# Optimization experiments

Measured on AMD Instinct MI355X. Metric: run time of the kernel, lower is better.

Reference implementation:

```python
import jax, jax.numpy as jnp
import numpy as np

NEG_SLOPE = 0.2


def gat_layer(x, src, dst, W, a_src, a_dst, num_nodes):
    """One PyG-style GATConv (self-loops already appended to src/dst).
    Returns [N, H, C] head-separated output (no bias/concat applied)."""
    H, C = a_src.shape
    h = (x @ W).reshape(num_nodes, H, C)            # [N,H,C]
    alpha_src = jnp.einsum('nhc,hc->nh', h, a_src)  # [N,H]
    alpha_dst = jnp.einsum('nhc,hc->nh', h, a_dst)  # [N,H]
    e = jax.nn.leaky_relu(alpha_src[src] + alpha_dst[dst], NEG_SLOPE)  # [E,H]
    # segment softmax over edges sharing the same destination node
    m = jax.ops.segment_max(e, dst, num_segments=num_nodes)[dst]
    ex = jnp.exp(e - m)
    denom = jax.ops.segment_sum(ex, dst, num_segments=num_nodes)[dst]
    alpha = ex / denom                               # [E,H]
    msg = h[src] * alpha[:, :, None]                 # [E,H,C]
    return jax.ops.segment_sum(msg, dst, num_segments=num_nodes)  # [N,H,C]


def setup_inputs() -> dict:
    key = jax.random.key(0)
    ks = jax.random.split(key, 10)
    N, E, IN, HID, OUT, H = 50000, 800000, 128, 32, 32, 4
    s = 0.1
    return {
        'x': jax.random.normal(ks[0], (N, IN), jnp.float32),
        'edge_index': jax.random.randint(ks[1], (2, E), 0, N, jnp.int64),
        'W1': jax.random.normal(ks[2], (IN, H * HID), jnp.float32) * s,
        'att_src1': jax.random.normal(ks[3], (H, HID), jnp.float32) * s,
        'att_dst1': jax.random.normal(ks[4], (H, HID), jnp.float32) * s,
        'b1': jax.random.normal(ks[5], (H * HID,), jnp.float32) * s,
        'W2': jax.random.normal(ks[6], (H * HID, OUT), jnp.float32) * s,
        'att_src2': jax.random.normal(ks[7], (1, OUT), jnp.float32) * s,
        'att_dst2': jax.random.normal(ks[8], (1, OUT), jnp.float32) * s,
        'b2': jax.random.normal(ks[9], (OUT,), jnp.float32) * s,
    }


def reference(x, edge_index, W1, att_src1, att_dst1, b1, W2, att_src2, att_dst2, b2):
    N = x.shape[0]
    # add self loops (PyG GATConv default)
    loop = jnp.arange(N, dtype=edge_index.dtype)
    src = jnp.concatenate([edge_index[0], loop])
    dst = jnp.concatenate([edge_index[1], loop])
    # layer 1: heads=4, concat=True
    h1 = gat_layer(x, src, dst, W1, att_src1, att_dst1, N).reshape(N, -1) + b1
    h1 = jax.nn.elu(h1)
    # layer 2: heads=1, concat=False -> mean over heads
    h2 = gat_layer(h1, src, dst, W2, att_src2, att_dst2, N).mean(axis=1) + b2
    return h2
```

## Files before the change

kernel.cpp:

```cpp
#include <hip/hip_runtime.h>
#include <math.h>

#define NEG_SLOPE 0.2f
typedef unsigned int uint;
typedef __attribute__((ext_vector_type(8))) short short8;
typedef __attribute__((ext_vector_type(4))) float floatx4;

__device__ __forceinline__ float lrelu(float x){ return x > 0.f ? x : NEG_SLOPE*x; }
__device__ __forceinline__ float sel4(float a,float b,float c,float d,int comp){
    return comp==0 ? a : (comp==1 ? b : (comp==2 ? c : d));
}
__device__ __forceinline__ uint f2bf(float f){
    uint u = __float_as_uint(f);
    return (u + 0x7FFFu + ((u>>16)&1u)) >> 16;
}
__device__ __forceinline__ float bf_lo(uint u){ return __uint_as_float(u<<16); }
__device__ __forceinline__ float bf_hi(uint u){ return __uint_as_float(u & 0xFFFF0000u); }
__device__ __forceinline__ float cexp(float x){ return __expf(fminf(x, 60.f)); }

__global__ __launch_bounds__(256) void k_prep(const float* __restrict__ W,
                                              ushort* __restrict__ wtb,
                                              int* __restrict__ offs, int N, int Etot)
{
    if (blockIdx.x == 0 && threadIdx.x == 0) offs[N] = Etot;
    int flat = blockIdx.x*1024 + threadIdx.x*4;
    int k = flat >> 7, c = flat & 127;
    float4 wv = *(const float4*)&W[flat];
    wtb[(size_t)(c+0)*128 + k] = (ushort)f2bf(wv.x);
    wtb[(size_t)(c+1)*128 + k] = (ushort)f2bf(wv.y);
    wtb[(size_t)(c+2)*128 + k] = (ushort)f2bf(wv.z);
    wtb[(size_t)(c+3)*128 + k] = (ushort)f2bf(wv.w);
}

__global__ __launch_bounds__(512) void k_g1b(const float* __restrict__ x,
    const ushort* __restrict__ wtb, uint* __restrict__ hb2, int N, int GB,
    const int* __restrict__ ei, int* __restrict__ bh, int E, int Etot, int NC, int NB)
{
    if (blockIdx.x >= GB){
        __shared__ uint hist[256];
        int c = blockIdx.x - GB;
        if (threadIdx.x < 256) hist[threadIdx.x] = 0;
        __syncthreads();
        int e0 = c*4096;
        #pragma unroll
        for (int r=0;r<8;r++){
            int e = e0 + r*512 + threadIdx.x;
            if (e < Etot){
                int d = (e < E) ? ei[E+e] : (e-E);
                atomicAdd(&hist[d>>8], 1u);
            }
        }
        __syncthreads();
        int b = threadIdx.x;
        if (b < NB) bh[(size_t)b*NC + c] = (int)hist[b];
        return;
    }
    __shared__ __align__(16) ushort xt[64][136];
    const int tid = threadIdx.x;
    const int row0 = blockIdx.x * 64;
    #pragma unroll
    for (int j=0;j<4;j++){
        int flat = j*2048 + tid*4;
        int r = flat >> 7, c = flat & 127;
        int gr = row0 + r;
        float4 xv = (gr < N) ? *(const float4*)&x[(size_t)gr*128 + c]
                             : make_float4(0.f,0.f,0.f,0.f);
        uint2 p;
        p.x = f2bf(xv.x) | (f2bf(xv.y)<<16);
        p.y = f2bf(xv.z) | (f2bf(xv.w)<<16);
        *(uint2*)&xt[r][c] = p;
    }
    __syncthreads();
    const int wv_ = tid >> 6, lane = tid & 63;
    const int l15 = lane & 15, hi = lane >> 4;
    const int rw = wv_ & 3, ch = wv_ >> 2;
    const int arow = rw*16 + l15;
    floatx4 acc[4];
    #pragma unroll
    for (int t=0;t<4;t++) acc[t] = (floatx4){0.f,0.f,0.f,0.f};
    #pragma unroll
    for (int ks=0; ks<4; ks++){
        short8 a = *(short8*)&xt[arow][ks*32 + hi*8];
        #pragma unroll
        for (int c4=0; c4<4; c4++){
            int ct = ch*4 + c4;
            short8 b = *(const short8*)&wtb[(size_t)(ct*16 + l15)*128 + ks*32 + hi*8];
            acc[c4] = __builtin_amdgcn_mfma_f32_16x16x32_bf16(a, b, acc[c4], 0, 0, 0);
        }
    }
    #pragma unroll
    for (int c4=0; c4<4; c4++){
        int ct = ch*4 + c4;
        #pragma unroll
        for (int r=0;r<4;r++){
            float v  = acc[c4][r];
            float pr = __shfl_xor(v, 1);
            int gr = row0 + rw*16 + (hi<<2) + r;
            if (((lane & 1) == 0) && gr < N)
                hb2[(size_t)gr*64 + ct*8 + (l15>>1)] = f2bf(v) | (f2bf(pr)<<16);
        }
    }
}

__global__ __launch_bounds__(256) void k_a1sc(const uint* __restrict__ hb2,
        const float* __restrict__ at_s, const float* __restrict__ at_d,
        float* __restrict__ as1, float* __restrict__ ad1, int N, int AB,
        const int* __restrict__ bh, int* __restrict__ bhs, int* __restrict__ partials2, int T)
{
    __shared__ int sm[256];
    if (blockIdx.x >= AB){
        int bid = blockIdx.x - AB;
        int tid = threadIdx.x;
        int i = bid*256 + tid;
        int v = (i < T) ? bh[i] : 0;
        sm[tid] = v;
        __syncthreads();
        for (int d=1; d<256; d<<=1){
            int t = (tid >= d) ? sm[tid-d] : 0;
            __syncthreads();
            sm[tid] += t;
            __syncthreads();
        }
        if (i < T) bhs[i] = sm[tid] - v;
        if (tid == 255) partials2[bid] = sm[255];
        return;
    }
    int wid = (blockIdx.x << 2) + (threadIdx.x >> 6);
    int lane = threadIdx.x & 63;
    if (wid >= N) return;
    uint hv = hb2[(size_t)wid*64 + lane];
    float f0 = bf_lo(hv), f1 = bf_hi(hv);
    float2 asv = *(const float2*)&at_s[2*lane];
    float2 adv = *(const float2*)&at_d[2*lane];
    float sa = f0*asv.x + f1*asv.y;
    float da = f0*adv.x + f1*adv.y;
    #pragma unroll
    for (int d=8; d>=1; d>>=1){ sa += __shfl_xor(sa,d); da += __shfl_xor(da,d); }
    if ((lane & 15) == 0){
        int head = lane >> 4;
        as1[(size_t)wid*4 + head] = sa;
        ad1[(size_t)wid*4 + head] = da;
    }
}

__global__ void k_bscan2s(int* __restrict__ bhs, const int* __restrict__ bh, int T){
    if (threadIdx.x == 0){
        int run = 0;
        for (int i=0;i<T;i++){ bhs[i] = run; run += bh[i]; }
    }
}

__global__ __launch_bounds__(256) void k_bscat(const int* __restrict__ ei,
        const int* __restrict__ bhs, const int* __restrict__ partials2, int L1e,
        uint* __restrict__ epack, int E, int Etot, int NC, int NB)
{
    __shared__ int sm[256];
    __shared__ int pbase[256];
    __shared__ uint cnt[256];
    int c = blockIdx.x, tid = threadIdx.x;
    int v = (tid < L1e) ? partials2[tid] : 0;
    sm[tid] = v;
    __syncthreads();
    for (int d=1; d<256; d<<=1){
        int t = (tid >= d) ? sm[tid-d] : 0;
        __syncthreads();
        sm[tid] += t;
        __syncthreads();
    }
    if (tid < NB){
        int i = tid*NC + c;
        int boff = (L1e == 0 || (i>>8) == 0) ? 0 : sm[(i>>8)-1];
        pbase[tid] = bhs[i] + boff;
    }
    cnt[tid] = 0;
    __syncthreads();
    int e0 = c*4096;
    #pragma unroll
    for (int r=0;r<16;r++){
        int e = e0 + r*256 + tid;
        if (e < Etot){
            int d, s;
            if (e < E){ s = ei[e]; d = ei[E+e]; }
            else      { s = e - E; d = e - E; }
            int b = d >> 8;
            uint lr = atomicAdd(&cnt[b], 1u);
            epack[pbase[b] + (int)lr] = (uint)s | ((uint)(d & 255) << 16);
        }
    }
}

__global__ __launch_bounds__(256) void k_bfin(const uint* __restrict__ epack,
        const int* __restrict__ bhs, const int* __restrict__ partials2, int L1e,
        int* __restrict__ bsrc, int* __restrict__ offs, int N, int NB, int NC, int Etot)
{
    __shared__ int sm[256];
    __shared__ int cnt[256], lofs[256], cnt2[256];
    int b = blockIdx.x, tid = threadIdx.x;
    int v = (tid < L1e) ? partials2[tid] : 0;
    sm[tid] = v;
    __syncthreads();
    for (int d=1; d<256; d<<=1){
        int t = (tid >= d) ? sm[tid-d] : 0;
        __syncthreads();
        sm[tid] += t;
        __syncthreads();
    }
    int i0 = b*NC;
    int start = bhs[i0] + ((L1e==0 || (i0>>8)==0) ? 0 : sm[(i0>>8)-1]);
    int end;
    if (b+1 < NB){
        int i1 = (b+1)*NC;
        end = bhs[i1] + ((L1e==0 || (i1>>8)==0) ? 0 : sm[(i1>>8)-1]);
    } else end = Etot;
    __syncthreads();
    cnt[tid] = 0; cnt2[tid] = 0;
    __syncthreads();
    for (int e = start + tid; e < end; e += 256)
        atomicAdd((uint*)&cnt[(epack[e] >> 16) & 255], 1u);
    __syncthreads();
    int v2 = cnt[tid];
    sm[tid] = v2;
    __syncthreads();
    for (int d=1; d<256; d<<=1){
        int t = (tid >= d) ? sm[tid-d] : 0;
        __syncthreads();
        sm[tid] += t;
        __syncthreads();
    }
    lofs[tid] = sm[tid] - v2;
    int nd = b*256 + tid;
    if (nd <= N) offs[nd] = start + sm[tid] - v2;
    __syncthreads();
    for (int e = start + tid; e < end; e += 256){
        uint u = epack[e];
        int dl = (u >> 16) & 255;
        int r = (int)atomicAdd((uint*)&cnt2[dl], 1u);
        bsrc[start + lofs[dl] + r] = (int)(u & 0xFFFFu);
    }
}

__global__ __launch_bounds__(512) void k_agg1(const uint* __restrict__ hb2,
    const float4* __restrict__ as1v, const float4* __restrict__ ad1v,
    const int* __restrict__ offs, const int* __restrict__ bsrc,
    const float* __restrict__ b1, float* __restrict__ exb,
    uint* __restrict__ hb1, int N)
{
    __shared__ float wsh[8][64][4];
    __shared__ int   ssh[8][64];
    int wv   = threadIdx.x >> 6;
    int wid  = (blockIdx.x << 3) + wv;
    int lane = threadIdx.x & 63;
    if (wid >= N) return;
    int base = offs[wid];
    int deg  = offs[wid+1] - base;
    float4 adv = ad1v[wid];
    const int comp = lane >> 4;
    float acc0=0.f, acc1=0.f;

    if (deg <= 64){
        const bool act = lane < deg;
        int sreg = 0;
        float e0=0.f,e1=0.f,e2=0.f,e3=0.f;
        if (act){
            sreg = bsrc[base+lane];
            float4 av = as1v[sreg];
            e0=cexp(lrelu(av.x+adv.x)); e1=cexp(lrelu(av.y+adv.y));
            e2=cexp(lrelu(av.z+adv.z)); e3=cexp(lrelu(av.w+adv.w));
        }
        float s0=e0,s1=e1,s2=e2,s3=e3;
        #pragma unroll
        for (int d=32; d>=1; d>>=1){
            s0+=__shfl_xor(s0,d); s1+=__shfl_xor(s1,d);
            s2+=__shfl_xor(s2,d); s3+=__shfl_xor(s3,d);
        }
        if (act){
            float i0=__builtin_amdgcn_rcpf(s0), i1=__builtin_amdgcn_rcpf(s1);
            float i2=__builtin_amdgcn_rcpf(s2), i3=__builtin_amdgcn_rcpf(s3);
            ssh[wv][lane]    = sreg << 6;
            wsh[wv][lane][0] = e0*i0;
            wsh[wv][lane][1] = e1*i1;
            wsh[wv][lane][2] = e2*i2;
            wsh[wv][lane][3] = e3*i3;
        }
        int j=0;
        for (; j+7 < deg; j+=8){
            uint o0=ssh[wv][j+0]+lane, o1=ssh[wv][j+1]+lane;
            uint o2=ssh[wv][j+2]+lane, o3=ssh[wv][j+3]+lane;
            uint o4=ssh[wv][j+4]+lane, o5=ssh[wv][j+5]+lane;
            uint o6=ssh[wv][j+6]+lane, o7=ssh[wv][j+7]+lane;
            float w0=wsh[wv][j+0][comp], w1=wsh[wv][j+1][comp];
            float w2=wsh[wv][j+2][comp], w3=wsh[wv][j+3][comp];
            float w4=wsh[wv][j+4][comp], w5=wsh[wv][j+5][comp];
            float w6=wsh[wv][j+6][comp], w7=wsh[wv][j+7][comp];
            uint h0=hb2[o0], h1_=hb2[o1], h2_=hb2[o2], h3=hb2[o3];
            uint h4=hb2[o4], h5=hb2[o5], h6=hb2[o6], h7=hb2[o7];
            acc0 = fmaf(bf_lo(h0), w0, acc0); acc1 = fmaf(bf_hi(h0), w0, acc1);
            acc0 = fmaf(bf_lo(h1_),w1, acc0); acc1 = fmaf(bf_hi(h1_),w1, acc1);
            acc0 = fmaf(bf_lo(h2_),w2, acc0); acc1 = fmaf(bf_hi(h2_),w2, acc1);
            acc0 = fmaf(bf_lo(h3), w3, acc0); acc1 = fmaf(bf_hi(h3), w3, acc1);
            acc0 = fmaf(bf_lo(h4), w4, acc0); acc1 = fmaf(bf_hi(h4), w4, acc1);
            acc0 = fmaf(bf_lo(h5), w5, acc0); acc1 = fmaf(bf_hi(h5), w5, acc1);
            acc0 = fmaf(bf_lo(h6), w6, acc0); acc1 = fmaf(bf_hi(h6), w6, acc1);
            acc0 = fmaf(bf_lo(h7), w7, acc0); acc1 = fmaf(bf_hi(h7), w7, acc1);
        }
        for (; j+3 < deg; j+=4){
            uint oA=ssh[wv][j]+lane,   oB=ssh[wv][j+1]+lane;
            uint oC=ssh[wv][j+2]+lane, oD=ssh[wv][j+3]+lane;
            float wA=wsh[wv][j][comp],   wB=wsh[wv][j+1][comp];
            float wC=wsh[wv][j+2][comp], wD=wsh[wv][j+3][comp];
            uint hA=hb2[oA], hB=hb2[oB], hC=hb2[oC], hD=hb2[oD];
            acc0 = fmaf(bf_lo(hA), wA, acc0); acc1 = fmaf(bf_hi(hA), wA, acc1);
            acc0 = fmaf(bf_lo(hB), wB, acc0); acc1 = fmaf(bf_hi(hB), wB, acc1);
            acc0 = fmaf(bf_lo(hC), wC, acc0); acc1 = fmaf(bf_hi(hC), wC, acc1);
            acc0 = fmaf(bf_lo(hD), wD, acc0); acc1 = fmaf(bf_hi(hD), wD, acc1);
        }
        for (; j < deg; j++){
            uint oA = ssh[wv][j]+lane;
            float wA = wsh[wv][j][comp];
            uint hA = hb2[oA];
            acc0 = fmaf(bf_lo(hA), wA, acc0);
            acc1 = fmaf(bf_hi(hA), wA, acc1);
        }
    } else {
        float s0=0,s1=0,s2=0,s3=0;
        for (int j=lane; j<deg; j+=64){
            int s = bsrc[base+j];
            float4 av = as1v[s];
            float e0=cexp(lrelu(av.x+adv.x));
            float e1=cexp(lrelu(av.y+adv.y));
            float e2=cexp(lrelu(av.z+adv.z));
            float e3=cexp(lrelu(av.w+adv.w));
            s0+=e0; s1+=e1; s2+=e2; s3+=e3;
            *(float4*)&exb[(size_t)(base+j)*4] = make_float4(e0,e1,e2,e3);
        }
        #pragma unroll
        for (int d=32; d>=1; d>>=1){
            s0+=__shfl_xor(s0,d); s1+=__shfl_xor(s1,d);
            s2+=__shfl_xor(s2,d); s3+=__shfl_xor(s3,d);
        }
        float invc = 1.0f / sel4(s0,s1,s2,s3,comp);
        for (int j=0;j<deg;j++){
            int s = bsrc[base+j];
            float w = exb[(size_t)(base+j)*4 + comp]*invc;
            uint hv = hb2[((uint)s<<6)+lane];
            acc0 = fmaf(bf_lo(hv), w, acc0);
            acc1 = fmaf(bf_hi(hv), w, acc1);
        }
    }
    float2 bv = *(const float2*)&b1[2*lane];
    float r0 = acc0 + bv.x;
    float r1 = acc1 + bv.y;
    r0 = r0 > 0.f ? r0 : (__expf(r0) - 1.f);
    r1 = r1 > 0.f ? r1 : (__expf(r1) - 1.f);
    hb1[(size_t)wid*64 + lane] = f2bf(r0) | (f2bf(r1)<<16);
}

__global__ __launch_bounds__(512) void k_l2pre(const uint* __restrict__ hb1,
    const float* __restrict__ W2, const float* __restrict__ asrc2,
    const float* __restrict__ adst2, uint* __restrict__ h2b,
    float* __restrict__ as2, float* __restrict__ ad2, int N)
{
    __shared__ __align__(16) float w2s[4096];
    __shared__ float a2s[32], a2d[32];
    int tid = threadIdx.x;
    #pragma unroll
    for (int q=0;q<2;q++){
        int idx = q*2048 + tid*4;
        *(float4*)&w2s[idx] = *(const float4*)&W2[idx];
    }
    if (tid < 32){ a2s[tid] = asrc2[tid]; a2d[tid] = adst2[tid]; }
    __syncthreads();
    int node = blockIdx.x*16 + (tid>>5);
    if (node >= N) return;
    int c = tid & 31;
    float acc = 0.f;
    #pragma unroll
    for (int k=0;k<128;k+=8){
        uint4 u = *(const uint4*)&hb1[(size_t)node*64 + (k>>1)];
        acc = fmaf(bf_lo(u.x), w2s[(k+0)*32+c], acc);
        acc = fmaf(bf_hi(u.x), w2s[(k+1)*32+c], acc);
        acc = fmaf(bf_lo(u.y), w2s[(k+2)*32+c], acc);
        acc = fmaf(bf_hi(u.y), w2s[(k+3)*32+c], acc);
        acc = fmaf(bf_lo(u.z), w2s[(k+4)*32+c], acc);
        acc = fmaf(bf_hi(u.z), w2s[(k+5)*32+c], acc);
        acc = fmaf(bf_lo(u.w), w2s[(k+6)*32+c], acc);
        acc = fmaf(bf_hi(u.w), w2s[(k+7)*32+c], acc);
    }
    float pr = __shfl_xor(acc, 1);
    if ((c & 1) == 0)
        h2b[(size_t)node*16 + (c>>1)] = f2bf(acc) | (f2bf(pr)<<16);
    float ps = acc * a2s[c], pd = acc * a2d[c];
    #pragma unroll
    for (int d=16; d>=1; d>>=1){ ps += __shfl_xor(ps,d); pd += __shfl_xor(pd,d); }
    if (c == 0){ as2[node] = ps; ad2[node] = pd; }
}

__global__ __launch_bounds__(512) void k_agg2(const uint* __restrict__ h2b,
    const float* __restrict__ as2, const float* __restrict__ ad2,
    const int* __restrict__ offs, const int* __restrict__ bsrc,
    const float* __restrict__ b2, float* __restrict__ exb,
    float* __restrict__ outp, int N)
{
    __shared__ float w2sh[8][64];
    __shared__ int   s2sh[8][64];
    int wv   = threadIdx.x >> 6;
    int wid  = (blockIdx.x << 3) + wv;
    int lane = threadIdx.x & 63;
    if (wid >= N) return;
    int base = offs[wid], deg = offs[wid+1] - base;
    float adn = ad2[wid];
    const int c2 = lane & 15, slot = lane >> 4;
    float acc0 = 0.f, acc1 = 0.f;

    if (deg <= 64){
        const bool act = lane < deg;
        int sreg = 0; float e = 0.f;
        if (act){ sreg = bsrc[base+lane]; e = cexp(lrelu(as2[sreg] + adn)); }
        float sum = e;
        #pragma unroll
        for (int d=32; d>=1; d>>=1) sum += __shfl_xor(sum,d);
        if (act){
            s2sh[wv][lane] = sreg << 4;
            w2sh[wv][lane] = e * __builtin_amdgcn_rcpf(sum);
        }
        int j = slot;
        for (; j+4 < deg; j += 8){
            uint oA = (uint)(s2sh[wv][j] + c2);
            uint oB = (uint)(s2sh[wv][j+4] + c2);
            float wA = w2sh[wv][j], wB = w2sh[wv][j+4];
            uint uA = h2b[oA], uB = h2b[oB];
            acc0 = fmaf(bf_lo(uA), wA, acc0); acc1 = fmaf(bf_hi(uA), wA, acc1);
            acc0 = fmaf(bf_lo(uB), wB, acc0); acc1 = fmaf(bf_hi(uB), wB, acc1);
        }
        for (; j < deg; j += 4){
            uint o  = (uint)(s2sh[wv][j] + c2);
            float w = w2sh[wv][j];
            uint u = h2b[o];
            acc0 = fmaf(bf_lo(u), w, acc0);
            acc1 = fmaf(bf_hi(u), w, acc1);
        }
    } else {
        float sum = 0.f;
        for (int j=lane; j<deg; j+=64){
            int s = bsrc[base+j];
            float ex = cexp(lrelu(as2[s] + adn));
            sum += ex;
            exb[base+j] = ex;
        }
        #pragma unroll
        for (int d=32; d>=1; d>>=1) sum += __shfl_xor(sum,d);
        float inv = 1.f/sum;
        for (int j=slot; j<deg; j+=4){
            int s  = bsrc[base+j];
            float w = exb[base+j]*inv;
            uint u = h2b[((uint)s<<4) + c2];
            acc0 = fmaf(bf_lo(u), w, acc0);
            acc1 = fmaf(bf_hi(u), w, acc1);
        }
    }
    acc0 += __shfl_xor(acc0, 16); acc0 += __shfl_xor(acc0, 32);
    acc1 += __shfl_xor(acc1, 16); acc1 += __shfl_xor(acc1, 32);
    if (lane < 16){
        float2 bv = *(const float2*)&b2[2*c2];
        *(float2*)&outp[(size_t)wid*32 + 2*c2] = make_float2(acc0 + bv.x, acc1 + bv.y);
    }
}

extern "C" void kernel_launch(void* const* d_in, const int* in_sizes, int n_in,
                              void* d_out, int out_size, void* d_ws, size_t ws_size,
                              hipStream_t stream)
{
    const float* x     = (const float*)d_in[0];
    const int*   ei    = (const int*)d_in[1];
    const float* W1    = (const float*)d_in[2];
    const float* at_s1 = (const float*)d_in[3];
    const float* at_d1 = (const float*)d_in[4];
    const float* b1    = (const float*)d_in[5];
    const float* W2    = (const float*)d_in[6];
    const float* at_s2 = (const float*)d_in[7];
    const float* at_d2 = (const float*)d_in[8];
    const float* b2    = (const float*)d_in[9];
    float* outp = (float*)d_out;

    const int N = in_sizes[0] / 128;
    const int E = in_sizes[1] / 2;
    const int Etot = E + N;

    const int NB = (N + 255) >> 8;
    const int NC = (Etot + 4095) / 4096;
    const int T  = NB * NC;
    const int L1 = (T + 255) / 256;

    float* f = (float*)d_ws;
    size_t off = 0;
    uint*  hb2 = (uint*)(f + off); off += (size_t)N*64;
    uint*  hb1 = (uint*)(f + off); off += (size_t)N*64;
    float* exb = f + off; off += (size_t)Etot*4;
    float* as1 = f + off; off += (size_t)N*4;
    float* ad1 = f + off; off += (size_t)N*4;
    uint*  h2b = (uint*)(f + off); off += (size_t)N*16;
    float* as2 = f + off; off += (size_t)N;
    float* ad2 = f + off; off += (size_t)N;
    ushort* wtb = (ushort*)(f + off); off += 8192;
    int* ib       = (int*)(f + off);
    int* offs     = ib;
    int* bh       = ib + N + 8;
    int* bhs      = bh + T;
    int* partials2= bhs + T;
    uint* epack   = (uint*)(partials2 + 256);
    int* bsrc     = (int*)(epack + Etot);

    const int GB = (N+63)/64;
    const int AB = (N+3)/4;

    k_prep <<<16, 256, 0, stream>>>(W1, wtb, offs, N, Etot);
    k_g1b  <<<GB+NC, 512, 0, stream>>>(x, wtb, hb2, N, GB, ei, bh, E, Etot, NC, NB);
    k_a1sc <<<AB+L1, 256, 0, stream>>>(hb2, at_s1, at_d1, as1, ad1, N, AB,
                                       bh, bhs, partials2, T);
    if (L1 <= 256){
        k_bscat<<<NC, 256, 0, stream>>>(ei, bhs, partials2, L1, epack, E, Etot, NC, NB);
        k_bfin <<<NB, 256, 0, stream>>>(epack, bhs, partials2, L1, bsrc, offs, N, NB, NC, Etot);
    } else {
        k_bscan2s<<<1, 1, 0, stream>>>(bhs, bh, T);
        k_bscat<<<NC, 256, 0, stream>>>(ei, bhs, partials2, 0, epack, E, Etot, NC, NB);
        k_bfin <<<NB, 256, 0, stream>>>(epack, bhs, partials2, 0, bsrc, offs, N, NB, NC, Etot);
    }
    k_agg1 <<<(N+7)/8, 512, 0, stream>>>(hb2, (const float4*)as1, (const float4*)ad1,
                                         offs, bsrc, b1, exb, hb1, N);
    k_l2pre<<<(N+15)/16, 512, 0, stream>>>(hb1, W2, at_s2, at_d2, h2b, as2, ad2, N);
    k_agg2 <<<(N+7)/8, 512, 0, stream>>>(h2b, as2, ad2, offs, bsrc, b2, exb, outp, N);
}
```

Measured before the change: 146.6 us.

## Store CSR source indices as ushort, prefetch W fragments, unroll agg1 gather by 16

Changes the sorted source-index array from int to ushort, halving its write in k_bfin and its reads in both aggregation kernels. In the GEMM kernel, the W bf16 fragments are loaded into registers before the barrier so their latency overlaps the x staging. The k_agg1 gather loop gains a 16-wide unrolled stage so more hb2 loads are in flight at once. The ushort indices depend on N staying below 65536, which the epack packing already assumed, and the wider unroll and register-held fragments raise register pressure.

Measured after the change: 146.2 us. About the same (-0.3%).

```diff
diff --git a/kernel.cpp b/kernel.cpp
--- a/kernel.cpp
+++ b/kernel.cpp
@@ -58,6 +58,10 @@
     __shared__ __align__(16) ushort xt[64][136];
     const int tid = threadIdx.x;
     const int row0 = blockIdx.x * 64;
+    const int wv_ = tid >> 6, lane = tid & 63;
+    const int l15 = lane & 15, hi = lane >> 4;
+    const int rw = wv_ & 3, ch = wv_ >> 2;
+    const int arow = rw*16 + l15;
     #pragma unroll
     for (int j=0;j<4;j++){
         int flat = j*2048 + tid*4;
@@ -70,11 +74,13 @@
         p.y = f2bf(xv.z) | (f2bf(xv.w)<<16);
         *(uint2*)&xt[r][c] = p;
     }
-    __syncthreads();
-    const int wv_ = tid >> 6, lane = tid & 63;
-    const int l15 = lane & 15, hi = lane >> 4;
-    const int rw = wv_ & 3, ch = wv_ >> 2;
-    const int arow = rw*16 + l15;
+    short8 bfrag[4][4];
+    #pragma unroll
+    for (int ks=0; ks<4; ks++)
+        #pragma unroll
+        for (int c4=0; c4<4; c4++)
+            bfrag[ks][c4] = *(const short8*)&wtb[(size_t)((ch*4+c4)*16 + l15)*128 + ks*32 + hi*8];
+    __syncthreads();
     floatx4 acc[4];
     #pragma unroll
     for (int t=0;t<4;t++) acc[t] = (floatx4){0.f,0.f,0.f,0.f};
@@ -82,11 +88,8 @@
     for (int ks=0; ks<4; ks++){
         short8 a = *(short8*)&xt[arow][ks*32 + hi*8];
         #pragma unroll
-        for (int c4=0; c4<4; c4++){
-            int ct = ch*4 + c4;
-            short8 b = *(const short8*)&wtb[(size_t)(ct*16 + l15)*128 + ks*32 + hi*8];
-            acc[c4] = __builtin_amdgcn_mfma_f32_16x16x32_bf16(a, b, acc[c4], 0, 0, 0);
-        }
+        for (int c4=0; c4<4; c4++)
+            acc[c4] = __builtin_amdgcn_mfma_f32_16x16x32_bf16(a, bfrag[ks][c4], acc[c4], 0, 0, 0);
     }
     #pragma unroll
     for (int c4=0; c4<4; c4++){
@@ -191,7 +194,7 @@
 
 __global__ __launch_bounds__(256) void k_bfin(const uint* __restrict__ epack,
         const int* __restrict__ bhs, const int* __restrict__ partials2, int L1e,
-        int* __restrict__ bsrc, int* __restrict__ offs, int N, int NB, int NC, int Etot)
+        ushort* __restrict__ bsrc, int* __restrict__ offs, int N, int NB, int NC, int Etot)
 {
     __shared__ int sm[256];
     __shared__ int cnt[256], lofs[256], cnt2[256];
@@ -235,13 +238,13 @@
         uint u = epack[e];
         int dl = (u >> 16) & 255;
         int r = (int)atomicAdd((uint*)&cnt2[dl], 1u);
-        bsrc[start + lofs[dl] + r] = (int)(u & 0xFFFFu);
+        bsrc[start + lofs[dl] + r] = (ushort)(u & 0xFFFFu);
     }
 }
 
 __global__ __launch_bounds__(512) void k_agg1(const uint* __restrict__ hb2,
     const float4* __restrict__ as1v, const float4* __restrict__ ad1v,
-    const int* __restrict__ offs, const int* __restrict__ bsrc,
+    const int* __restrict__ offs, const ushort* __restrict__ bsrc,
     const float* __restrict__ b1, float* __restrict__ exb,
     uint* __restrict__ hb1, int N)
 {
@@ -262,7 +265,7 @@
         int sreg = 0;
         float e0=0.f,e1=0.f,e2=0.f,e3=0.f;
         if (act){
-            sreg = bsrc[base+lane];
+            sreg = (int)bsrc[base+lane];
             float4 av = as1v[sreg];
             e0=cexp(lrelu(av.x+adv.x)); e1=cexp(lrelu(av.y+adv.y));
             e2=cexp(lrelu(av.z+adv.z)); e3=cexp(lrelu(av.w+adv.w));
@@ -283,39 +286,44 @@
             wsh[wv][lane][3] = e3*i3;
         }
         int j=0;
+        for (; j+15 < deg; j+=16){
+            uint o[16], h[16]; float w[16];
+            #pragma unroll
+            for (int q=0;q<16;q++) o[q] = (uint)ssh[wv][j+q] + lane;
+            #pragma unroll
+            for (int q=0;q<16;q++){ h[q] = hb2[o[q]]; w[q] = wsh[wv][j+q][comp]; }
+            #pragma unroll
+            for (int q=0;q<16;q++){
+                acc0 = fmaf(bf_lo(h[q]), w[q], acc0);
+                acc1 = fmaf(bf_hi(h[q]), w[q], acc1);
+            }
+        }
         for (; j+7 < deg; j+=8){
-            uint o0=ssh[wv][j+0]+lane, o1=ssh[wv][j+1]+lane;
-            uint o2=ssh[wv][j+2]+lane, o3=ssh[wv][j+3]+lane;
-            uint o4=ssh[wv][j+4]+lane, o5=ssh[wv][j+5]+lane;
-            uint o6=ssh[wv][j+6]+lane, o7=ssh[wv][j+7]+lane;
-            float w0=wsh[wv][j+0][comp], w1=wsh[wv][j+1][comp];
-            float w2=wsh[wv][j+2][comp], w3=wsh[wv][j+3][comp];
-            float w4=wsh[wv][j+4][comp], w5=wsh[wv][j+5][comp];
-            float w6=wsh[wv][j+6][comp], w7=wsh[wv][j+7][comp];
-            uint h0=hb2[o0], h1_=hb2[o1], h2_=hb2[o2], h3=hb2[o3];
-            uint h4=hb2[o4], h5=hb2[o5], h6=hb2[o6], h7=hb2[o7];
-            acc0 = fmaf(bf_lo(h0), w0, acc0); acc1 = fmaf(bf_hi(h0), w0, acc1);
-            acc0 = fmaf(bf_lo(h1_),w1, acc0); acc1 = fmaf(bf_hi(h1_),w1, acc1);
-            acc0 = fmaf(bf_lo(h2_),w2, acc0); acc1 = fmaf(bf_hi(h2_),w2, acc1);
-            acc0 = fmaf(bf_lo(h3), w3, acc0); acc1 = fmaf(bf_hi(h3), w3, acc1);
-            acc0 = fmaf(bf_lo(h4), w4, acc0); acc1 = fmaf(bf_hi(h4), w4, acc1);
-            acc0 = fmaf(bf_lo(h5), w5, acc0); acc1 = fmaf(bf_hi(h5), w5, acc1);
-            acc0 = fmaf(bf_lo(h6), w6, acc0); acc1 = fmaf(bf_hi(h6), w6, acc1);
-            acc0 = fmaf(bf_lo(h7), w7, acc0); acc1 = fmaf(bf_hi(h7), w7, acc1);
+            uint o[8], h[8]; float w[8];
+            #pragma unroll
+            for (int q=0;q<8;q++) o[q] = (uint)ssh[wv][j+q] + lane;
+            #pragma unroll
+            for (int q=0;q<8;q++){ h[q] = hb2[o[q]]; w[q] = wsh[wv][j+q][comp]; }
+            #pragma unroll
+            for (int q=0;q<8;q++){
+                acc0 = fmaf(bf_lo(h[q]), w[q], acc0);
+                acc1 = fmaf(bf_hi(h[q]), w[q], acc1);
+            }
         }
         for (; j+3 < deg; j+=4){
-            uint oA=ssh[wv][j]+lane,   oB=ssh[wv][j+1]+lane;
-            uint oC=ssh[wv][j+2]+lane, oD=ssh[wv][j+3]+lane;
-            float wA=wsh[wv][j][comp],   wB=wsh[wv][j+1][comp];
-            float wC=wsh[wv][j+2][comp], wD=wsh[wv][j+3][comp];
-            uint hA=hb2[oA], hB=hb2[oB], hC=hb2[oC], hD=hb2[oD];
-            acc0 = fmaf(bf_lo(hA), wA, acc0); acc1 = fmaf(bf_hi(hA), wA, acc1);
-            acc0 = fmaf(bf_lo(hB), wB, acc0); acc1 = fmaf(bf_hi(hB), wB, acc1);
-            acc0 = fmaf(bf_lo(hC), wC, acc0); acc1 = fmaf(bf_hi(hC), wC, acc1);
-            acc0 = fmaf(bf_lo(hD), wD, acc0); acc1 = fmaf(bf_hi(hD), wD, acc1);
+            uint o[4], h[4]; float w[4];
+            #pragma unroll
+            for (int q=0;q<4;q++) o[q] = (uint)ssh[wv][j+q] + lane;
+            #pragma unroll
+            for (int q=0;q<4;q++){ h[q] = hb2[o[q]]; w[q] = wsh[wv][j+q][comp]; }
+            #pragma unroll
+            for (int q=0;q<4;q++){
+                acc0 = fmaf(bf_lo(h[q]), w[q], acc0);
+                acc1 = fmaf(bf_hi(h[q]), w[q], acc1);
+            }
         }
         for (; j < deg; j++){
-            uint oA = ssh[wv][j]+lane;
+            uint oA = (uint)ssh[wv][j] + lane;
             float wA = wsh[wv][j][comp];
             uint hA = hb2[oA];
             acc0 = fmaf(bf_lo(hA), wA, acc0);
@@ -324,7 +332,7 @@
     } else {
         float s0=0,s1=0,s2=0,s3=0;
         for (int j=lane; j<deg; j+=64){
-            int s = bsrc[base+j];
+            int s = (int)bsrc[base+j];
             float4 av = as1v[s];
             float e0=cexp(lrelu(av.x+adv.x));
             float e1=cexp(lrelu(av.y+adv.y));
@@ -340,7 +348,7 @@
         }
         float invc = 1.0f / sel4(s0,s1,s2,s3,comp);
         for (int j=0;j<deg;j++){
-            int s = bsrc[base+j];
+            int s = (int)bsrc[base+j];
             float w = exb[(size_t)(base+j)*4 + comp]*invc;
             uint hv = hb2[((uint)s<<6)+lane];
             acc0 = fmaf(bf_lo(hv), w, acc0);
@@ -397,7 +405,7 @@
 
 __global__ __launch_bounds__(512) void k_agg2(const uint* __restrict__ h2b,
     const float* __restrict__ as2, const float* __restrict__ ad2,
-    const int* __restrict__ offs, const int* __restrict__ bsrc,
+    const int* __restrict__ offs, const ushort* __restrict__ bsrc,
     const float* __restrict__ b2, float* __restrict__ exb,
     float* __restrict__ outp, int N)
 {
@@ -415,7 +423,7 @@
     if (deg <= 64){
         const bool act = lane < deg;
         int sreg = 0; float e = 0.f;
-        if (act){ sreg = bsrc[base+lane]; e = cexp(lrelu(as2[sreg] + adn)); }
+        if (act){ sreg = (int)bsrc[base+lane]; e = cexp(lrelu(as2[sreg] + adn)); }
         float sum = e;
         #pragma unroll
         for (int d=32; d>=1; d>>=1) sum += __shfl_xor(sum,d);
@@ -442,7 +450,7 @@
     } else {
         float sum = 0.f;
         for (int j=lane; j<deg; j+=64){
-            int s = bsrc[base+j];
+            int s = (int)bsrc[base+j];
             float ex = cexp(lrelu(as2[s] + adn));
             sum += ex;
             exb[base+j] = ex;
@@ -451,7 +459,7 @@
         for (int d=32; d>=1; d>>=1) sum += __shfl_xor(sum,d);
         float inv = 1.f/sum;
         for (int j=slot; j<deg; j+=4){
-            int s  = bsrc[base+j];
+            int s  = (int)bsrc[base+j];
             float w = exb[base+j]*inv;
             uint u = h2b[((uint)s<<4) + c2];
             acc0 = fmaf(bf_lo(u), w, acc0);
@@ -508,7 +516,7 @@
     int* bhs      = bh + T;
     int* partials2= bhs + T;
     uint* epack   = (uint*)(partials2 + 256);
-    int* bsrc     = (int*)(epack + Etot);
+    ushort* bsrc  = (ushort*)(epack + Etot);
 
     const int GB = (N+63)/64;
     const int AB = (N+3)/4;
```
